# Kernel tuning notes

Hardware: AMD Instinct MI355X
Metric: run time of the kernel (lower is better)

The kernel has to match this reference:

```python
import jax, jax.numpy as jnp
import numpy as np

EPS = 1e-5
K = 20

def knn(x, k):
    # x: (B, 3, N) -> idx (B, N, k) of nearest neighbors (negative sq-dist topk)
    inner = -2.0 * jnp.einsum('bcn,bcm->bnm', x, x)
    xx = jnp.sum(x * x, axis=1)  # (B, N)
    pd = -xx[:, :, None] - inner - xx[:, None, :]
    return jax.lax.top_k(pd, k)[1]

def graph_feature(feats, idx):
    # feats: (B, C, N), idx: (B, N, k) -> (B, 2C, N, k)
    ft = jnp.transpose(feats, (0, 2, 1))  # (B, N, C)
    gathered = jax.vmap(lambda f, i: f[i])(ft, idx)  # (B, N, k, C)
    center = ft[:, :, None, :]  # (B, N, 1, C)
    out = jnp.concatenate([gathered - center,
                           jnp.broadcast_to(center, gathered.shape)], axis=3)
    return jnp.transpose(out, (0, 3, 1, 2))  # (B, 2C, N, k)

def bn2d(h, g, b):
    m = jnp.mean(h, axis=(0, 2, 3), keepdims=True)
    v = jnp.var(h, axis=(0, 2, 3), keepdims=True)
    return (h - m) * jax.lax.rsqrt(v + EPS) * g[None, :, None, None] + b[None, :, None, None]

def bn1d(h, g, b):
    m = jnp.mean(h, axis=(0, 2), keepdims=True)
    v = jnp.var(h, axis=(0, 2), keepdims=True)
    return (h - m) * jax.lax.rsqrt(v + EPS) * g[None, :, None] + b[None, :, None]

def edge_block(x, feats, w, g, b):
    idx = knn(x, K)
    ef = graph_feature(feats, idx)                  # (B, 2C, N, k)
    h = jnp.einsum('bcnk,oc->bonk', ef, w)          # 1x1 conv, no bias
    h = jnp.tanh(bn2d(h, g, b))
    return jnp.max(h, axis=-1)                      # (B, O, N)


def setup_inputs() -> dict:
    key = jax.random.key(0)
    ks = jax.random.split(key, 20)
    B, N, FD, EMB = 8, 2048, 3, 1024
    def w_init(k, o, i):
        return jax.random.normal(k, (o, i), dtype=jnp.float32) * (1.0 / np.sqrt(i))
    inp = {
        'x': jax.random.normal(ks[0], (B, N, 3), dtype=jnp.float32),
        'features': jax.random.normal(ks[1], (B, N, FD), dtype=jnp.float32),
        'w1': w_init(ks[2], 64, 2 * FD),
        'g1': jnp.ones((64,), jnp.float32), 'b1': jnp.zeros((64,), jnp.float32),
        'w2': w_init(ks[3], 64, 128),
        'g2': jnp.ones((64,), jnp.float32), 'b2': jnp.zeros((64,), jnp.float32),
        'w3': w_init(ks[4], 128, 128),
        'g3': jnp.ones((128,), jnp.float32), 'b3': jnp.zeros((128,), jnp.float32),
        'w4': w_init(ks[5], 256, 256),
        'g4': jnp.ones((256,), jnp.float32), 'b4': jnp.zeros((256,), jnp.float32),
        'w5': w_init(ks[6], EMB, 512),
        'g5': jnp.ones((EMB,), jnp.float32), 'b5': jnp.zeros((EMB,), jnp.float32),
    }
    return inp


def reference(x, features, w1, g1, b1, w2, g2, b2, w3, g3, b3, w4, g4, b4, w5, g5, b5):
    xt = jnp.transpose(x, (0, 2, 1))          # (B, 3, N)
    ft = jnp.transpose(features, (0, 2, 1))   # (B, FD, N)
    B = xt.shape[0]
    f1 = edge_block(xt, ft, w1, g1, b1)       # (B, 64, N)
    f2 = edge_block(xt, f1, w2, g2, b2)       # (B, 64, N)
    f3 = edge_block(xt, f2, w3, g3, b3)       # (B, 128, N)
    f4 = edge_block(xt, f3, w4, g4, b4)       # (B, 256, N)
    cat = jnp.concatenate([f1, f2, f3, f4], axis=1)   # (B, 512, N)
    f5 = jnp.tanh(bn1d(jnp.einsum('bcn,oc->bon', cat, w5), g5, b5))  # (B, EMB, N)
    mx = jnp.max(f5, axis=-1)
    av = jnp.mean(f5, axis=-1)
    return jnp.concatenate([mx, av], axis=1)  # (B, 2*EMB)
```

## Files before the change

kernel.cpp:

```cpp
#include <hip/hip_runtime.h>
#include <cstdio>
#include <cstdint>

#define NPTS 2048
#define NB   8
#define KK   20

typedef __attribute__((ext_vector_type(8))) short  short8;
typedef __attribute__((ext_vector_type(8))) unsigned short ushort8;
typedef __attribute__((ext_vector_type(4))) float  f32x4;
typedef unsigned short ushort;
typedef unsigned int   uint;

#define AS1 __attribute__((address_space(1)))
#define AS3 __attribute__((address_space(3)))

__device__ __forceinline__ ushort f2bf(float f) {
    uint u = __float_as_uint(f);
    u += 0x7fffu + ((u >> 16) & 1u);
    return (ushort)(u >> 16);
}
__device__ __forceinline__ float bf2f(ushort s) { return __uint_as_float((uint)s << 16); }

__device__ __forceinline__ void gload16(const ushort* g, ushort* l) {
    __builtin_amdgcn_global_load_lds((const AS1 uint*)(const void*)g,
                                     (AS3 uint*)(void*)l, 16, 0, 0);
}

__global__ __launch_bounds__(512) void knn_kernel(const float* __restrict__ x,
                                                  int* __restrict__ idx)
{
    __shared__ float4 sp[NPTS];
    const int tid = threadIdx.x;
    const int wv = tid >> 6, lane = tid & 63;
    const int gn0 = blockIdx.x * 8;
    const int b = gn0 >> 11;
    const float* xb = x + (size_t)b * NPTS * 3;

    for (int p = tid; p < NPTS; p += 512) {
        const float a0 = xb[p * 3 + 0], a1 = xb[p * 3 + 1], a2 = xb[p * 3 + 2];
        sp[p] = make_float4(a0, a1, a2, a0 * a0 + a1 * a1 + a2 * a2);
    }
    __syncthreads();

    const int n = (gn0 & (NPTS - 1)) + wv;
    const float4 pn = sp[n];
    const float xxn = pn.w;

    float d[32];
#pragma unroll
    for (int i = 0; i < 32; ++i) {
        const float4 pm = sp[lane + i * 64];
        const float dot = pm.x * pn.x + pm.y * pn.y + pm.z * pn.z;
        const float inner = -2.0f * dot;
        d[i] = (-xxn - inner) - pm.w;
    }

    float gv[4]; int gs[4];
#pragma unroll
    for (int g = 0; g < 4; ++g) {
        float v = d[g * 8]; int s = 0;
#pragma unroll
        for (int j = 1; j < 8; ++j)
            if (d[g * 8 + j] > v) { v = d[g * 8 + j]; s = j; }
        gv[g] = v; gs[g] = s;
    }

    int* op = idx + ((size_t)b * NPTS + n) * KK;
    for (int it = 0; it < KK; ++it) {
        float bv = gv[0]; int bm8 = gs[0];
#pragma unroll
        for (int g = 1; g < 4; ++g)
            if (gv[g] > bv) { bv = gv[g]; bm8 = g * 8 + gs[g]; }
        const int m = lane + (bm8 << 6);

        const uint u = __float_as_uint(bv);
        const uint r = (u & 0x80000000u) ? ~u : (u | 0x80000000u);
        unsigned long long key =
            ((unsigned long long)r << 11) | (unsigned)(2047 - m);

#pragma unroll
        for (int s2 = 32; s2; s2 >>= 1) {
            const unsigned long long ok =
                (unsigned long long)__shfl_xor((long long)key, s2);
            key = (ok > key) ? ok : key;
        }
        const int mw = 2047 - (int)(key & 2047u);
        if (lane == 0) op[it] = mw;

        const int mws   = __builtin_amdgcn_readfirstlane(mw);
        const int wslot = mws >> 6;
        const int wgrp  = wslot >> 3;
        const int wj    = wslot & 7;
        const bool iswin = (lane == (mws & 63));

#pragma unroll
        for (int G = 0; G < 4; ++G) {
            if (wgrp == G) {
#pragma unroll
                for (int j = 0; j < 8; ++j)
                    if (j == wj) d[G * 8 + j] = iswin ? -1e38f : d[G * 8 + j];
                float v = d[G * 8]; int s = 0;
#pragma unroll
                for (int j = 1; j < 8; ++j)
                    if (d[G * 8 + j] > v) { v = d[G * 8 + j]; s = j; }
                gv[G] = v; gs[G] = s;
            }
        }
    }
}

__global__ __launch_bounds__(256) void y1_kernel(const float* __restrict__ feats,
                                                 const float* __restrict__ w1,
                                                 float* __restrict__ Y)
{
    __shared__ float w[384];
    const int tid = threadIdx.x;
    for (int i = tid; i < 384; i += 256) w[i] = w1[i];
    __syncthreads();

    const int b  = blockIdx.y;
    const int p  = blockIdx.x * 2 + (tid >> 7);
    const int o2 = tid & 127;
    const int o = o2 & 63, half = o2 >> 6;
    const float* fp = feats + ((size_t)b * NPTS + p) * 3;
    const float f0 = fp[0], f1 = fp[1], f2 = fp[2];
    const float* wr = &w[o * 6 + half * 3];
    Y[((size_t)b * NPTS + p) * 128 + o2] = wr[0] * f0 + wr[1] * f1 + wr[2] * f2;
}

__global__ __launch_bounds__(256) void wsplit_kernel(const float* __restrict__ w2,
                                                     const float* __restrict__ w3,
                                                     const float* __restrict__ w4,
                                                     ushort* q2h, ushort* q2l,
                                                     ushort* q3h, ushort* q3l,
                                                     ushort* q4h, ushort* q4l)
{
    const int t = blockIdx.x * 256 + threadIdx.x;
    float v; ushort *dh, *dl; int off;
    if (t < 8192)        { int i = t;         int m = i >> 6, c = i & 63;  int o = m & 63,  hf = m >> 6; v = w2[o * 128 + hf * 64  + c]; dh = q2h; dl = q2l; off = i; }
    else if (t < 24576)  { int i = t - 8192;  int m = i >> 6, c = i & 63;  int o = m & 127, hf = m >> 7; v = w3[o * 128 + hf * 64  + c]; dh = q3h; dl = q3l; off = i; }
    else if (t < 90112)  { int i = t - 24576; int m = i >> 7, c = i & 127; int o = m & 255, hf = m >> 8; v = w4[o * 256 + hf * 128 + c]; dh = q4h; dl = q4l; off = i; }
    else return;
    const ushort h = f2bf(v);
    dh[off] = h;
    dl[off] = f2bf(v - bf2f(h));
}

__global__ __launch_bounds__(256) void wsplit5_kernel(const float* __restrict__ w5,
                                                      ushort* q5h, ushort* q5l)
{
    const int t = blockIdx.x * 256 + threadIdx.x;
    if (t >= 1024 * 512) return;
    const float v = w5[t];
    const ushort h = f2bf(v);
    q5h[t] = h;
    q5l[t] = f2bf(v - bf2f(h));
}

template<bool PF32, bool STATS, bool SWZ>
__global__ __launch_bounds__(256) void gemm_mfma(const float* __restrict__ Pf,
                                                 const ushort* __restrict__ Ph,
                                                 const ushort* __restrict__ Pl,
                                                 const ushort* __restrict__ Qh,
                                                 const ushort* __restrict__ Ql,
                                                 float* __restrict__ Out,
                                                 double* __restrict__ est,
                                                 int K, int pitchP, int pitchQ, int ldO,
                                                 long strideP, long strideQ, long strideO)
{
    constexpr int PH = 0, PL = 4096, QH = 8192, QL = 12288;
    constexpr int BUF = 16384;
    __shared__ ushort lds_buf[32768];

    const int tid  = threadIdx.x;
    const int wv   = tid >> 6, lane = tid & 63;

    int bx, by, bz;
    if constexpr (SWZ) {
        const int id = blockIdx.x;
        const int J  = (id & 7) * 128 + (id >> 3);
        bx = J & 7; by = (J >> 3) & 15; bz = J >> 7;
    } else { bx = blockIdx.x; by = blockIdx.y; bz = blockIdx.z; }

    const int i0   = bx * 128;
    const int j0   = by * 128;
    const long prow0 = (long)bz * strideP + (long)i0 * pitchP;
    const long qrow0 = (long)bz * strideQ + (long)j0 * pitchQ;

    const int iw = (wv >> 1) * 64;
    const int jw = (wv & 1) * 64;
    const int lr = lane & 15;
    const int lc = lane >> 4;

    f32x4 acc[4][4];
#pragma unroll
    for (int f = 0; f < 4; ++f)
#pragma unroll
        for (int g = 0; g < 4; ++g) acc[f][g] = (f32x4){0.f, 0.f, 0.f, 0.f};

    auto STAGE = [&](int k0, int bb) {
        const int r16 = lane >> 2;
        const int cp  = lane & 3;
#pragma unroll
        for (int q = 0; q < 2; ++q) {
            const int row = wv * 32 + q * 16 + r16;
            const int cl  = cp ^ ((row >> 1) & 3);
            const long go = (long)row * pitchQ + k0 + cl * 8;
            gload16(Qh + qrow0 + go, &lds_buf[bb + QH + (wv * 32 + q * 16) * 32]);
            gload16(Ql + qrow0 + go, &lds_buf[bb + QL + (wv * 32 + q * 16) * 32]);
        }
        if constexpr (!PF32) {
#pragma unroll
            for (int q = 0; q < 2; ++q) {
                const int row = wv * 32 + q * 16 + r16;
                const int cl  = cp ^ ((row >> 1) & 3);
                const long go = (long)row * pitchP + k0 + cl * 8;
                gload16(Ph + prow0 + go, &lds_buf[bb + PH + (wv * 32 + q * 16) * 32]);
                gload16(Pl + prow0 + go, &lds_buf[bb + PL + (wv * 32 + q * 16) * 32]);
            }
        } else {
#pragma unroll
            for (int r = 0; r < 2; ++r) {
                const int id2 = r * 256 + tid;
                const int row = id2 >> 2, cl = id2 & 3;
                const int cpw = cl ^ ((row >> 1) & 3);
                const float* gp = Pf + prow0 + (long)row * pitchP + k0 + cl * 8;
                const float4 v0 = *(const float4*)gp;
                const float4 v1 = *(const float4*)(gp + 4);
                const float vv[8] = {v0.x, v0.y, v0.z, v0.w, v1.x, v1.y, v1.z, v1.w};
                ushort8 hi, lo;
#pragma unroll
                for (int e2 = 0; e2 < 8; ++e2) {
                    const ushort h = f2bf(vv[e2]);
                    hi[e2] = h;
                    lo[e2] = f2bf(vv[e2] - bf2f(h));
                }
                *(ushort8*)&lds_buf[bb + PH + row * 32 + cpw * 8] = hi;
                *(ushort8*)&lds_buf[bb + PL + row * 32 + cpw * 8] = lo;
            }
        }
    };

    const int NT  = K >> 5;
    const int cpa = lc ^ ((lr >> 1) & 3);
    int bb = 0;

    STAGE(0, 0);

    for (int t = 0; t < NT; ++t) {
        if (t + 1 < NT) {
            STAGE((t + 1) << 5, bb ^ BUF);
            if constexpr (PF32)
                asm volatile("s_waitcnt vmcnt(0) lgkmcnt(0)" ::: "memory");
            else
                asm volatile("s_waitcnt vmcnt(8)" ::: "memory");
        } else {
            asm volatile("s_waitcnt vmcnt(0) lgkmcnt(0)" ::: "memory");
        }
        __builtin_amdgcn_s_barrier();
        __builtin_amdgcn_sched_barrier(0);

        short8 ah[4], al[4], bh[4], bl[4];
#pragma unroll
        for (int f = 0; f < 4; ++f) {
            const int ra = (iw + f * 16 + lr) * 32 + cpa * 8;
            ah[f] = *(const short8*)&lds_buf[bb + PH + ra];
            al[f] = *(const short8*)&lds_buf[bb + PL + ra];
            const int rb = (jw + f * 16 + lr) * 32 + cpa * 8;
            bh[f] = *(const short8*)&lds_buf[bb + QH + rb];
            bl[f] = *(const short8*)&lds_buf[bb + QL + rb];
        }
#pragma unroll
        for (int f = 0; f < 4; ++f)
#pragma unroll
            for (int g = 0; g < 4; ++g) {
                acc[f][g] = __builtin_amdgcn_mfma_f32_16x16x32_bf16(ah[f], bh[g], acc[f][g], 0, 0, 0);
                acc[f][g] = __builtin_amdgcn_mfma_f32_16x16x32_bf16(ah[f], bl[g], acc[f][g], 0, 0, 0);
                acc[f][g] = __builtin_amdgcn_mfma_f32_16x16x32_bf16(al[f], bh[g], acc[f][g], 0, 0, 0);
            }

        __builtin_amdgcn_s_barrier();
        bb ^= BUF;
    }

    const long ob = (long)bz * strideO;
#pragma unroll
    for (int f = 0; f < 4; ++f) {
        const int i = i0 + iw + f * 16 + lc * 4;
#pragma unroll
        for (int g = 0; g < 4; ++g) {
            const int j = j0 + jw + g * 16 + lr;
#pragma unroll
            for (int r = 0; r < 4; ++r)
                Out[ob + (long)(i + r) * ldO + j] = acc[f][g][r];
        }
    }

    if constexpr (STATS) {
        const int slab = blockIdx.x & 7;
#pragma unroll
        for (int f = 0; f < 4; ++f)
#pragma unroll
            for (int r = 0; r < 4; ++r) {
                float s = 0.f, s2 = 0.f;
#pragma unroll
                for (int g = 0; g < 4; ++g) {
                    const float v = acc[f][g][r];
                    s += v;
                    s2 = fmaf(v, v, s2);
                }
#pragma unroll
                for (int d2 = 1; d2 <= 8; d2 <<= 1) {
                    s  += __shfl_xor(s, d2);
                    s2 += __shfl_xor(s2, d2);
                }
                if (lr == 0) {
                    const int i = i0 + iw + f * 16 + lc * 4 + r;
                    atomicAdd(&est[(size_t)slab * 2048 + i],        (double)s);
                    atomicAdd(&est[(size_t)slab * 2048 + 1024 + i], (double)s2);
                }
            }
    }
}

template<int O, int NCH>
__global__ __launch_bounds__(256) void edge_apply(const float* __restrict__ Y,
                                                  const int* __restrict__ knn_idx,
                                                  float* __restrict__ mx_out,
                                                  double* __restrict__ st)
{
    constexpr int M = 2 * O;
    constexpr int NPB = 256 / O;
    const int blk = blockIdx.x;
    const int b     = blk & 7;
    const int chunk = blk >> 3;
    const int tid = threadIdx.x;
    const int o   = tid & (O - 1);
    const int sub = tid / O;
    const int n0  = chunk * (NPB * NCH);
    const size_t rowb = (size_t)b * NPTS;
    float s = 0.f, s2 = 0.f;

#pragma unroll
    for (int it = 0; it < NCH; ++it) {
        const int n = n0 + it * NPB + sub;
        const float* yr = Y + (rowb + n) * M;
        const float base = yr[O + o] - yr[o];
        const int* ip = knn_idx + (rowb + n) * KK;
        int mm[KK];
#pragma unroll
        for (int j = 0; j < KK; ++j) mm[j] = ip[j];
        float h[KK];
#pragma unroll
        for (int j = 0; j < KK; ++j) h[j] = Y[(rowb + mm[j]) * M + o];
        float mx = -1e38f;
#pragma unroll
        for (int j = 0; j < KK; ++j) {
            const float v = h[j] + base;
            mx = fmaxf(mx, v);
            s += v;
            s2 = fmaf(v, v, s2);
        }
        mx_out[(rowb + n) * O + o] = mx;
    }
    double* stp = st + (size_t)(chunk & 7) * (2 * O);
    atomicAdd(&stp[o],     (double)s);
    atomicAdd(&stp[O + o], (double)s2);
}

template<int O>
__global__ __launch_bounds__(256) void edge_finalize(const float* __restrict__ mx_in,
                                                     const double* __restrict__ st,
                                                     const float* __restrict__ gamma,
                                                     const float* __restrict__ beta,
                                                     ushort* __restrict__ ch,
                                                     ushort* __restrict__ cl_,
                                                     int c0)
{
    __shared__ float ssc[256], ssh[256];
    const int b = blockIdx.y;
    const int tid = threadIdx.x;
    if (tid < O) {
        double ssum = 0.0, s2sum = 0.0;
#pragma unroll
        for (int sl = 0; sl < 8; ++sl) {
            ssum  += st[(size_t)sl * (2 * O) + tid];
            s2sum += st[(size_t)sl * (2 * O) + O + tid];
        }
        const double cnt = (double)NB * NPTS * KK;
        const double mean = ssum / cnt;
        const double var  = s2sum / cnt - mean * mean;
        const float rs = rsqrtf((float)var + 1e-5f);
        const float sc = gamma[tid] * rs;
        ssc[tid] = sc;
        ssh[tid] = beta[tid] - (float)mean * sc;
    }
    __syncthreads();

    const int o   = tid & (O - 1);
    const int sub = tid / O;
    const int n0  = blockIdx.x * 8;
    constexpr int NPB = 256 / O;
#pragma unroll
    for (int it = 0; it < 8 / NPB; ++it) {
        const int n = n0 + it * NPB + sub;
        const float v = mx_in[((size_t)b * NPTS + n) * O + o];
        const float f = tanhf(fmaf(v, ssc[o], ssh[o]));
        const ushort h = f2bf(f);
        const size_t co = ((size_t)b * NPTS + n) * 512 + c0 + o;
        ch[co]  = h;
        cl_[co] = f2bf(f - bf2f(h));
    }
}

__global__ __launch_bounds__(256) void final_kernel(const float* __restrict__ e,
                                                    const double* __restrict__ st,
                                                    const float* __restrict__ g5,
                                                    const float* __restrict__ b5,
                                                    float* __restrict__ out)
{
    const int b = blockIdx.y;
    const int wv = threadIdx.x >> 6, lane = threadIdx.x & 63;
    const int o = blockIdx.x * 4 + wv;
    double ssum = 0.0, s2sum = 0.0;
#pragma unroll
    for (int sl = 0; sl < 8; ++sl) {
        ssum  += st[(size_t)sl * 2048 + o];
        s2sum += st[(size_t)sl * 2048 + 1024 + o];
    }
    const double cnt = (double)NB * NPTS;
    const double mean = ssum / cnt;
    const double var  = s2sum / cnt - mean * mean;
    const float rs = rsqrtf((float)var + 1e-5f);
    const float sc = g5[o] * rs;
    const float sh = b5[o] - (float)mean * sc;
    const float* row = e + ((size_t)(b * 1024 + o)) * NPTS;
    float mx = -1e38f, sm = 0.f;
    for (int n = lane; n < NPTS; n += 64) {
        const float v = tanhf(fmaf(row[n], sc, sh));
        mx = fmaxf(mx, v);
        sm += v;
    }
#pragma unroll
    for (int d = 32; d > 0; d >>= 1) {
        mx = fmaxf(mx, __shfl_xor(mx, d));
        sm += __shfl_xor(sm, d);
    }
    if (lane == 0) {
        out[(size_t)b * 2048 + o]        = mx;
        out[(size_t)b * 2048 + 1024 + o] = sm * (1.0f / 2048.0f);
    }
}

extern "C" void kernel_launch(void* const* d_in, const int* in_sizes, int n_in,
                              void* d_out, int out_size, void* d_ws, size_t ws_size,
                              hipStream_t stream)
{
    (void)in_sizes; (void)n_in; (void)out_size;
    const float* x  = (const float*)d_in[0];
    const float* ft = (const float*)d_in[1];
    const float* w1 = (const float*)d_in[2];
    const float* g1 = (const float*)d_in[3];
    const float* b1 = (const float*)d_in[4];
    const float* w2 = (const float*)d_in[5];
    const float* g2 = (const float*)d_in[6];
    const float* b2 = (const float*)d_in[7];
    const float* w3 = (const float*)d_in[8];
    const float* g3 = (const float*)d_in[9];
    const float* b3 = (const float*)d_in[10];
    const float* w4 = (const float*)d_in[11];
    const float* g4 = (const float*)d_in[12];
    const float* b4 = (const float*)d_in[13];
    const float* w5 = (const float*)d_in[14];
    const float* g5 = (const float*)d_in[15];
    const float* b5 = (const float*)d_in[16];
    float* out = (float*)d_out;

    const size_t STATS_OFF = 0;
    const size_t ESTAT_OFF = 131072;
    const size_t IDX_OFF   = 262144;
    const size_t Q2H_OFF   = 1572864,  Q2L_OFF = 1589248;
    const size_t Q3H_OFF   = 1605632,  Q3L_OFF = 1638400;
    const size_t Q4H_OFF   = 1671168,  Q4L_OFF = 1802240;
    const size_t CTH_OFF   = 1933312;
    const size_t CTL_OFF   = 18710528;
    const size_t Y_OFF     = 35487744;
    const size_t MX_OFF    = 69042176;
    const size_t NEED_BASE = 102596608;
    const size_t Q5H_OFF   = 102596608, Q5L_OFF = 103645184;
    const size_t NEED_FULL = 104693760;
    if (ws_size < NEED_BASE) {
        fprintf(stderr, "kernel_launch: ws too small (%zu < %zu)\n", ws_size, NEED_BASE);
        return;
    }
    const bool presplit = (ws_size >= NEED_FULL);

    char* ws = (char*)d_ws;
    double* stats  = (double*)(ws + STATS_OFF);
    double* estats = (double*)(ws + ESTAT_OFF);
    int*    idx    = (int*)(ws + IDX_OFF);
    ushort* q2h = (ushort*)(ws + Q2H_OFF); ushort* q2l = (ushort*)(ws + Q2L_OFF);
    ushort* q3h = (ushort*)(ws + Q3H_OFF); ushort* q3l = (ushort*)(ws + Q3L_OFF);
    ushort* q4h = (ushort*)(ws + Q4H_OFF); ushort* q4l = (ushort*)(ws + Q4L_OFF);
    ushort* q5h = (ushort*)(ws + Q5H_OFF); ushort* q5l = (ushort*)(ws + Q5L_OFF);
    ushort* cth = (ushort*)(ws + CTH_OFF); ushort* ctl = (ushort*)(ws + CTL_OFF);
    float*  Y   = (float*)(ws + Y_OFF);
    float*  mxb = (float*)(ws + MX_OFF);
    float*  e   = (float*)(ws + Y_OFF);

    hipMemsetAsync(ws, 0, 262144, stream);

    knn_kernel<<<NB * NPTS / 8, 512, 0, stream>>>(x, idx);
    wsplit_kernel<<<352, 256, 0, stream>>>(w2, w3, w4, q2h, q2l, q3h, q3l, q4h, q4l);
    if (presplit)
        wsplit5_kernel<<<2048, 256, 0, stream>>>(w5, q5h, q5l);

    y1_kernel<<<dim3(NPTS / 2, NB), 256, 0, stream>>>(ft, w1, Y);
    edge_apply<64, 2><<<2048, 256, 0, stream>>>(Y, idx, mxb, stats + 0 * 4096);
    edge_finalize<64><<<dim3(256, NB), 256, 0, stream>>>(mxb, stats + 0 * 4096, g1, b1, cth, ctl, 0);

    gemm_mfma<false, false, false><<<dim3(16, 1, 8), 256, 0, stream>>>(
        nullptr, cth + 0, ctl + 0, q2h, q2l, Y, nullptr,
        64, 512, 64, 128, (long)NPTS * 512, 0, (long)NPTS * 128);
    edge_apply<64, 2><<<2048, 256, 0, stream>>>(Y, idx, mxb, stats + 1 * 4096);
    edge_finalize<64><<<dim3(256, NB), 256, 0, stream>>>(mxb, stats + 1 * 4096, g2, b2, cth, ctl, 64);

    gemm_mfma<false, false, false><<<dim3(16, 2, 8), 256, 0, stream>>>(
        nullptr, cth + 64, ctl + 64, q3h, q3l, Y, nullptr,
        64, 512, 64, 256, (long)NPTS * 512, 0, (long)NPTS * 256);
    edge_apply<128, 4><<<2048, 256, 0, stream>>>(Y, idx, mxb, stats + 2 * 4096);
    edge_finalize<128><<<dim3(256, NB), 256, 0, stream>>>(mxb, stats + 2 * 4096, g3, b3, cth, ctl, 128);

    gemm_mfma<false, false, false><<<dim3(16, 4, 8), 256, 0, stream>>>(
        nullptr, cth + 128, ctl + 128, q4h, q4l, Y, nullptr,
        128, 512, 128, 512, (long)NPTS * 512, 0, (long)NPTS * 512);
    edge_apply<256, 8><<<2048, 256, 0, stream>>>(Y, idx, mxb, stats + 3 * 4096);
    edge_finalize<256><<<dim3(256, NB), 256, 0, stream>>>(mxb, stats + 3 * 4096, g4, b4, cth, ctl, 256);

    if (presplit) {
        gemm_mfma<false, true, true><<<1024, 256, 0, stream>>>(
            nullptr, q5h, q5l, cth, ctl, e, estats,
            512, 512, 512, 2048, 0, (long)NPTS * 512, (long)1024 * 2048);
    } else {
        gemm_mfma<true, true, true><<<1024, 256, 0, stream>>>(
            w5, nullptr, nullptr, cth, ctl, e, estats,
            512, 512, 512, 2048, 0, (long)NPTS * 512, (long)1024 * 2048);
    }
    final_kernel<<<dim3(256, NB), 256, 0, stream>>>(e, estats, g5, b5, out);
}
```

Baseline: 377.2 us.

## Use 256x256 tiles with 512 threads for the final embedding GEMM

Adds a gemm_mfma256 kernel with 256x256 output tiles, 8 waves each computing 128x64, and twice the LDS double buffer, used for the large w5 GEMM with BN statistics. The old templated gemm is reduced to the small edge-conv GEMMs. Larger tiles halve global/LDS reloads per output and reuse B fragments across 8 A fragments, but launch only 256 blocks (about one per CU) with higher register pressure from 32 accumulators, which can lower occupancy and latency hiding.

Result: slower. 395.2 us (+4.8%).

```diff
diff --git a/kernel.cpp b/kernel.cpp
--- a/kernel.cpp
+++ b/kernel.cpp
@@ -158,14 +158,11 @@
     q5l[t] = f2bf(v - bf2f(h));
 }
 
-template<bool PF32, bool STATS, bool SWZ>
-__global__ __launch_bounds__(256) void gemm_mfma(const float* __restrict__ Pf,
-                                                 const ushort* __restrict__ Ph,
+__global__ __launch_bounds__(256) void gemm_mfma(const ushort* __restrict__ Ph,
                                                  const ushort* __restrict__ Pl,
                                                  const ushort* __restrict__ Qh,
                                                  const ushort* __restrict__ Ql,
                                                  float* __restrict__ Out,
-                                                 double* __restrict__ est,
                                                  int K, int pitchP, int pitchQ, int ldO,
                                                  long strideP, long strideQ, long strideO)
 {
@@ -176,15 +173,9 @@
     const int tid  = threadIdx.x;
     const int wv   = tid >> 6, lane = tid & 63;
 
-    int bx, by, bz;
-    if constexpr (SWZ) {
-        const int id = blockIdx.x;
-        const int J  = (id & 7) * 128 + (id >> 3);
-        bx = J & 7; by = (J >> 3) & 15; bz = J >> 7;
-    } else { bx = blockIdx.x; by = blockIdx.y; bz = blockIdx.z; }
-
-    const int i0   = bx * 128;
-    const int j0   = by * 128;
+    const int i0   = blockIdx.x * 128;
+    const int j0   = blockIdx.y * 128;
+    const int bz   = blockIdx.z;
     const long prow0 = (long)bz * strideP + (long)i0 * pitchP;
     const long qrow0 = (long)bz * strideQ + (long)j0 * pitchQ;
 
@@ -206,26 +197,130 @@
         for (int q = 0; q < 2; ++q) {
             const int row = wv * 32 + q * 16 + r16;
             const int cl  = cp ^ ((row >> 1) & 3);
-            const long go = (long)row * pitchQ + k0 + cl * 8;
-            gload16(Qh + qrow0 + go, &lds_buf[bb + QH + (wv * 32 + q * 16) * 32]);
-            gload16(Ql + qrow0 + go, &lds_buf[bb + QL + (wv * 32 + q * 16) * 32]);
-        }
-        if constexpr (!PF32) {
-#pragma unroll
-            for (int q = 0; q < 2; ++q) {
-                const int row = wv * 32 + q * 16 + r16;
-                const int cl  = cp ^ ((row >> 1) & 3);
-                const long go = (long)row * pitchP + k0 + cl * 8;
-                gload16(Ph + prow0 + go, &lds_buf[bb + PH + (wv * 32 + q * 16) * 32]);
-                gload16(Pl + prow0 + go, &lds_buf[bb + PL + (wv * 32 + q * 16) * 32]);
-            }
+            const long goq = (long)row * pitchQ + k0 + cl * 8;
+            gload16(Qh + qrow0 + goq, &lds_buf[bb + QH + (wv * 32 + q * 16) * 32]);
+            gload16(Ql + qrow0 + goq, &lds_buf[bb + QL + (wv * 32 + q * 16) * 32]);
+            const long gop = (long)row * pitchP + k0 + cl * 8;
+            gload16(Ph + prow0 + gop, &lds_buf[bb + PH + (wv * 32 + q * 16) * 32]);
+            gload16(Pl + prow0 + gop, &lds_buf[bb + PL + (wv * 32 + q * 16) * 32]);
+        }
+    };
+
+    const int NT  = K >> 5;
+    const int cpa = lc ^ ((lr >> 1) & 3);
+    int bb = 0;
+
+    STAGE(0, 0);
+
+    for (int t = 0; t < NT; ++t) {
+        if (t + 1 < NT) {
+            STAGE((t + 1) << 5, bb ^ BUF);
+            asm volatile("s_waitcnt vmcnt(8)" ::: "memory");
         } else {
+            asm volatile("s_waitcnt vmcnt(0) lgkmcnt(0)" ::: "memory");
+        }
+        __builtin_amdgcn_s_barrier();
+        __builtin_amdgcn_sched_barrier(0);
+
+        short8 ah[4], al[4], bh[4], bl[4];
+#pragma unroll
+        for (int f = 0; f < 4; ++f) {
+            const int ra = (iw + f * 16 + lr) * 32 + cpa * 8;
+            ah[f] = *(const short8*)&lds_buf[bb + PH + ra];
+            al[f] = *(const short8*)&lds_buf[bb + PL + ra];
+            const int rb = (jw + f * 16 + lr) * 32 + cpa * 8;
+            bh[f] = *(const short8*)&lds_buf[bb + QH + rb];
+            bl[f] = *(const short8*)&lds_buf[bb + QL + rb];
+        }
+#pragma unroll
+        for (int f = 0; f < 4; ++f)
+#pragma unroll
+            for (int g = 0; g < 4; ++g) {
+                acc[f][g] = __builtin_amdgcn_mfma_f32_16x16x32_bf16(ah[f], bh[g], acc[f][g], 0, 0, 0);
+                acc[f][g] = __builtin_amdgcn_mfma_f32_16x16x32_bf16(ah[f], bl[g], acc[f][g], 0, 0, 0);
+                acc[f][g] = __builtin_amdgcn_mfma_f32_16x16x32_bf16(al[f], bh[g], acc[f][g], 0, 0, 0);
+            }
+
+        __builtin_amdgcn_s_barrier();
+        bb ^= BUF;
+    }
+
+    const long ob = (long)bz * strideO;
+#pragma unroll
+    for (int f = 0; f < 4; ++f) {
+        const int i = i0 + iw + f * 16 + lc * 4;
+#pragma unroll
+        for (int g = 0; g < 4; ++g) {
+            const int j = j0 + jw + g * 16 + lr;
+#pragma unroll
+            for (int r = 0; r < 4; ++r)
+                Out[ob + (long)(i + r) * ldO + j] = acc[f][g][r];
+        }
+    }
+}
+
+template<bool PF32>
+__global__ __launch_bounds__(512) void gemm_mfma256(const float* __restrict__ Pf,
+                                                    const ushort* __restrict__ Ph,
+                                                    const ushort* __restrict__ Pl,
+                                                    const ushort* __restrict__ Qh,
+                                                    const ushort* __restrict__ Ql,
+                                                    float* __restrict__ Out,
+                                                    double* __restrict__ est,
+                                                    int K, int pitchP, int pitchQ, int ldO,
+                                                    long strideP, long strideQ, long strideO)
+{
+    constexpr int PH = 0, PL = 8192, QH = 16384, QL = 24576;
+    constexpr int BUF = 32768;
+    __shared__ ushort lds_buf[65536];
+
+    const int tid  = threadIdx.x;
+    const int wv   = tid >> 6, lane = tid & 63;
+
+    const int id = blockIdx.x;
+    const int J  = (id & 7) * 32 + (id >> 3);
+    const int bx = J & 3, by = (J >> 2) & 7, bz = J >> 5;
+
+    const int i0 = bx * 256;
+    const int j0 = by * 256;
+    const long prow0 = (long)bz * strideP + (long)i0 * pitchP;
+    const long qrow0 = (long)bz * strideQ + (long)j0 * pitchQ;
+
+    const int iw = (wv >> 2) * 128;
+    const int jw = (wv & 3) * 64;
+    const int lr = lane & 15;
+    const int lc = lane >> 4;
+
+    f32x4 acc[8][4];
+#pragma unroll
+    for (int f = 0; f < 8; ++f)
+#pragma unroll
+        for (int g = 0; g < 4; ++g) acc[f][g] = (f32x4){0.f, 0.f, 0.f, 0.f};
+
+    auto STAGE = [&](int k0, int bb) {
+        const int r16 = lane >> 2;
+        const int cp  = lane & 3;
+#pragma unroll
+        for (int q = 0; q < 2; ++q) {
+            const int grp = wv + q * 8;
+            const int row = grp * 16 + r16;
+            const int cl  = cp ^ ((row >> 1) & 3);
+            const long goq = (long)row * pitchQ + k0 + cl * 8;
+            gload16(Qh + qrow0 + goq, &lds_buf[bb + QH + grp * 512]);
+            gload16(Ql + qrow0 + goq, &lds_buf[bb + QL + grp * 512]);
+            if constexpr (!PF32) {
+                const long gop = (long)row * pitchP + k0 + cl * 8;
+                gload16(Ph + prow0 + gop, &lds_buf[bb + PH + grp * 512]);
+                gload16(Pl + prow0 + gop, &lds_buf[bb + PL + grp * 512]);
+            }
+        }
+        if constexpr (PF32) {
 #pragma unroll
             for (int r = 0; r < 2; ++r) {
-                const int id2 = r * 256 + tid;
-                const int row = id2 >> 2, cl = id2 & 3;
-                const int cpw = cl ^ ((row >> 1) & 3);
-                const float* gp = Pf + prow0 + (long)row * pitchP + k0 + cl * 8;
+                const int id2 = r * 512 + tid;
+                const int row = id2 >> 2, cl2 = id2 & 3;
+                const int cpw = cl2 ^ ((row >> 1) & 3);
+                const float* gp = Pf + prow0 + (long)row * pitchP + k0 + cl2 * 8;
                 const float4 v0 = *(const float4*)gp;
                 const float4 v1 = *(const float4*)(gp + 4);
                 const float vv[8] = {v0.x, v0.y, v0.z, v0.w, v1.x, v1.y, v1.z, v1.w};
@@ -261,24 +356,25 @@
         __builtin_amdgcn_s_barrier();
         __builtin_amdgcn_sched_barrier(0);
 
-        short8 ah[4], al[4], bh[4], bl[4];
-#pragma unroll
-        for (int f = 0; f < 4; ++f) {
+        short8 bh[4], bl[4];
+#pragma unroll
+        for (int g = 0; g < 4; ++g) {
+            const int rb = (jw + g * 16 + lr) * 32 + cpa * 8;
+            bh[g] = *(const short8*)&lds_buf[bb + QH + rb];
+            bl[g] = *(const short8*)&lds_buf[bb + QL + rb];
+        }
+#pragma unroll
+        for (int f = 0; f < 8; ++f) {
             const int ra = (iw + f * 16 + lr) * 32 + cpa * 8;
-            ah[f] = *(const short8*)&lds_buf[bb + PH + ra];
-            al[f] = *(const short8*)&lds_buf[bb + PL + ra];
-            const int rb = (jw + f * 16 + lr) * 32 + cpa * 8;
-            bh[f] = *(const short8*)&lds_buf[bb + QH + rb];
-            bl[f] = *(const short8*)&lds_buf[bb + QL + rb];
-        }
-#pragma unroll
-        for (int f = 0; f < 4; ++f)
+            const short8 ah = *(const short8*)&lds_buf[bb + PH + ra];
+            const short8 al = *(const short8*)&lds_buf[bb + PL + ra];
 #pragma unroll
             for (int g = 0; g < 4; ++g) {
-                acc[f][g] = __builtin_amdgcn_mfma_f32_16x16x32_bf16(ah[f], bh[g], acc[f][g], 0, 0, 0);
-                acc[f][g] = __builtin_amdgcn_mfma_f32_16x16x32_bf16(ah[f], bl[g], acc[f][g], 0, 0, 0);
-                acc[f][g] = __builtin_amdgcn_mfma_f32_16x16x32_bf16(al[f], bh[g], acc[f][g], 0, 0, 0);
-            }
+                acc[f][g] = __builtin_amdgcn_mfma_f32_16x16x32_bf16(ah, bh[g], acc[f][g], 0, 0, 0);
+                acc[f][g] = __builtin_amdgcn_mfma_f32_16x16x32_bf16(ah, bl[g], acc[f][g], 0, 0, 0);
+                acc[f][g] = __builtin_amdgcn_mfma_f32_16x16x32_bf16(al, bh[g], acc[f][g], 0, 0, 0);
+            }
+        }
 
         __builtin_amdgcn_s_barrier();
         bb ^= BUF;
@@ -286,7 +382,7 @@
 
     const long ob = (long)bz * strideO;
 #pragma unroll
-    for (int f = 0; f < 4; ++f) {
+    for (int f = 0; f < 8; ++f) {
         const int i = i0 + iw + f * 16 + lc * 4;
 #pragma unroll
         for (int g = 0; g < 4; ++g) {
@@ -297,31 +393,29 @@
         }
     }
 
-    if constexpr (STATS) {
-        const int slab = blockIdx.x & 7;
-#pragma unroll
-        for (int f = 0; f < 4; ++f)
-#pragma unroll
-            for (int r = 0; r < 4; ++r) {
-                float s = 0.f, s2 = 0.f;
-#pragma unroll
-                for (int g = 0; g < 4; ++g) {
-                    const float v = acc[f][g][r];
-                    s += v;
-                    s2 = fmaf(v, v, s2);
-                }
-#pragma unroll
-                for (int d2 = 1; d2 <= 8; d2 <<= 1) {
-                    s  += __shfl_xor(s, d2);
-                    s2 += __shfl_xor(s2, d2);
-                }
-                if (lr == 0) {
-                    const int i = i0 + iw + f * 16 + lc * 4 + r;
-                    atomicAdd(&est[(size_t)slab * 2048 + i],        (double)s);
-                    atomicAdd(&est[(size_t)slab * 2048 + 1024 + i], (double)s2);
-                }
-            }
-    }
+    const int slab = id & 7;
+#pragma unroll
+    for (int f = 0; f < 8; ++f)
+#pragma unroll
+        for (int r = 0; r < 4; ++r) {
+            float s = 0.f, s2 = 0.f;
+#pragma unroll
+            for (int g = 0; g < 4; ++g) {
+                const float v = acc[f][g][r];
+                s += v;
+                s2 = fmaf(v, v, s2);
+            }
+#pragma unroll
+            for (int d2 = 1; d2 <= 8; d2 <<= 1) {
+                s  += __shfl_xor(s, d2);
+                s2 += __shfl_xor(s2, d2);
+            }
+            if (lr == 0) {
+                const int i = i0 + iw + f * 16 + lc * 4 + r;
+                atomicAdd(&est[(size_t)slab * 2048 + i],        (double)s);
+                atomicAdd(&est[(size_t)slab * 2048 + 1024 + i], (double)s2);
+            }
+        }
 }
 
 template<int O, int NCH>
@@ -520,30 +614,30 @@
     edge_apply<64, 2><<<2048, 256, 0, stream>>>(Y, idx, mxb, stats + 0 * 4096);
     edge_finalize<64><<<dim3(256, NB), 256, 0, stream>>>(mxb, stats + 0 * 4096, g1, b1, cth, ctl, 0);
 
-    gemm_mfma<false, false, false><<<dim3(16, 1, 8), 256, 0, stream>>>(
-        nullptr, cth + 0, ctl + 0, q2h, q2l, Y, nullptr,
+    gemm_mfma<<<dim3(16, 1, 8), 256, 0, stream>>>(
+        cth + 0, ctl + 0, q2h, q2l, Y,
         64, 512, 64, 128, (long)NPTS * 512, 0, (long)NPTS * 128);
     edge_apply<64, 2><<<2048, 256, 0, stream>>>(Y, idx, mxb, stats + 1 * 4096);
     edge_finalize<64><<<dim3(256, NB), 256, 0, stream>>>(mxb, stats + 1 * 4096, g2, b2, cth, ctl, 64);
 
-    gemm_mfma<false, false, false><<<dim3(16, 2, 8), 256, 0, stream>>>(
-        nullptr, cth + 64, ctl + 64, q3h, q3l, Y, nullptr,
+    gemm_mfma<<<dim3(16, 2, 8), 256, 0, stream>>>(
+        cth + 64, ctl + 64, q3h, q3l, Y,
         64, 512, 64, 256, (long)NPTS * 512, 0, (long)NPTS * 256);
     edge_apply<128, 4><<<2048, 256, 0, stream>>>(Y, idx, mxb, stats + 2 * 4096);
     edge_finalize<128><<<dim3(256, NB), 256, 0, stream>>>(mxb, stats + 2 * 4096, g3, b3, cth, ctl, 128);
 
-    gemm_mfma<false, false, false><<<dim3(16, 4, 8), 256, 0, stream>>>(
-        nullptr, cth + 128, ctl + 128, q4h, q4l, Y, nullptr,
+    gemm_mfma<<<dim3(16, 4, 8), 256, 0, stream>>>(
+        cth + 128, ctl + 128, q4h, q4l, Y,
         128, 512, 128, 512, (long)NPTS * 512, 0, (long)NPTS * 512);
     edge_apply<256, 8><<<2048, 256, 0, stream>>>(Y, idx, mxb, stats + 3 * 4096);
     edge_finalize<256><<<dim3(256, NB), 256, 0, stream>>>(mxb, stats + 3 * 4096, g4, b4, cth, ctl, 256);
 
     if (presplit) {
-        gemm_mfma<false, true, true><<<1024, 256, 0, stream>>>(
+        gemm_mfma256<false><<<256, 512, 0, stream>>>(
             nullptr, q5h, q5l, cth, ctl, e, estats,
             512, 512, 512, 2048, 0, (long)NPTS * 512, (long)1024 * 2048);
     } else {
-        gemm_mfma<true, true, true><<<1024, 256, 0, stream>>>(
+        gemm_mfma256<true><<<256, 512, 0, stream>>>(
             w5, nullptr, nullptr, cth, ctl, e, estats,
             512, 512, 512, 2048, 0, (long)NPTS * 512, (long)1024 * 2048);
     }
```
